# Kernel tuning notes

Hardware: AMD Instinct MI355X
Metric: run time of the kernel (lower is better)

## Reference

```python
import jax, jax.numpy as jnp
import numpy as np

B, S, D = 4, 2048, 2048
H, Dh, Dl = 16, 128, 128  # head_dim must equal latent_dim for the source matmul to type-check


def setup_inputs() -> dict:
    key = jax.random.key(0)
    ks = jax.random.split(key, 6)
    sc = 0.02
    return {
        "hidden_states": jax.random.normal(ks[0], (B, S, D), dtype=jnp.float32),
        "Wq": jax.random.normal(ks[1], (H * Dh, D), dtype=jnp.float32) * sc,
        "Wk_down": jax.random.normal(ks[2], (H * Dl, D), dtype=jnp.float32) * sc,
        "Wv_down": jax.random.normal(ks[3], (H * Dl, D), dtype=jnp.float32) * sc,
        "Wk_up": jax.random.normal(ks[4], (H * Dh, H * Dl), dtype=jnp.float32) * sc,
        "Wo": jax.random.normal(ks[5], (D, H * Dh), dtype=jnp.float32) * sc,
    }


def reference(hidden_states, Wq, Wk_down, Wv_down, Wk_up, Wo):
    # projections (torch Linear: y = x @ W.T)
    q = (hidden_states @ Wq.T).reshape(B, S, H, Dh).transpose(0, 2, 1, 3)        # [B,H,S,Dh]
    k_lat = (hidden_states @ Wk_down.T).reshape(B, S, H, Dl).transpose(0, 2, 1, 3)  # [B,H,S,Dl]
    v_lat = (hidden_states @ Wv_down.T).reshape(B, S, H, Dl).transpose(0, 2, 1, 3)  # [B,H,S,Dl]

    scores = jnp.einsum("bhsd,bhtd->bhst", q, k_lat) / jnp.sqrt(jnp.float32(Dl))
    attn = jax.nn.softmax(scores, axis=-1)
    out_lat = jnp.einsum("bhst,bhtd->bhsd", attn, v_lat)                          # [B,H,S,Dl]
    out_lat = out_lat.transpose(0, 2, 1, 3).reshape(B, S, H * Dl)

    # source bug (faithful): k_up_proj is applied to the attention output
    up = out_lat @ Wk_up.T                                                         # [B,S,H*Dh]
    return up @ Wo.T                                                               # [B,S,D]
```

## Files before the change

kernel.cpp:

```cpp
#include <hip/hip_runtime.h>
#include <hip/hip_bf16.h>
#include <stdint.h>

typedef unsigned short u16;
typedef __attribute__((ext_vector_type(4))) float f32x4;
typedef __attribute__((ext_vector_type(8))) short s16x8;
typedef __attribute__((ext_vector_type(4))) u16 u16x4;

__device__ __forceinline__ u16 f2bf(float x) {
  union { float f; uint32_t u; } v; v.f = x;
  uint32_t r = v.u + 0x7FFFu + ((v.u >> 16) & 1u);
  return (u16)(r >> 16);
}
__device__ __forceinline__ u16 f2bfh(float x) {
  __hip_bfloat16 h = __float2bfloat16(x);
  u16 r; __builtin_memcpy(&r, &h, 2); return r;
}

__device__ __forceinline__ void gload16(const void* g, const void* l) {
  __builtin_amdgcn_global_load_lds((const __attribute__((address_space(1))) void*)g,
                                   (__attribute__((address_space(3))) void*)l,
                                   16, 0, 0);
}

#define BAR() asm volatile("s_barrier" ::: "memory")
#define VMCNT4() asm volatile("s_waitcnt vmcnt(4)" ::: "memory")
#define VMCNT0() asm volatile("s_waitcnt vmcnt(0)" ::: "memory")

__global__ void fill_k(float* out, int n, float v) {
  for (int i = blockIdx.x * blockDim.x + threadIdx.x; i < n; i += gridDim.x * blockDim.x)
    out[i] = v;
}

__global__ void cvtall_k(const float* __restrict__ hs, const float* __restrict__ Wq,
                         const float* __restrict__ Wkd, const float* __restrict__ Wvd,
                         const float* __restrict__ Wo,
                         u16* __restrict__ hsB, u16* __restrict__ W3, u16* __restrict__ WoB) {
  int i = blockIdx.x * blockDim.x + threadIdx.x;
  const float* src; u16* dst; int off;
  if (i < 4194304)      { src = hs;  dst = hsB;          off = i; }
  else if (i < 5242880) { src = Wq;  dst = W3;           off = i - 4194304; }
  else if (i < 6291456) { src = Wkd; dst = W3 + 4194304; off = i - 5242880; }
  else if (i < 7340032) { src = Wvd; dst = W3 + 8388608; off = i - 6291456; }
  else                  { src = Wo;  dst = WoB;          off = i - 7340032; }
  f32x4 v = ((const f32x4*)src)[off];
  u16x4 o;
  o.x = f2bf(v.x); o.y = f2bf(v.y); o.z = f2bf(v.z); o.w = f2bf(v.w);
  ((u16x4*)dst)[off] = o;
}

__global__ void cvtT_k(const float* __restrict__ in, u16* __restrict__ out) {
  __shared__ float t[32][33];
  int tx = threadIdx.x, ty = threadIdx.y;
  int c = blockIdx.x * 32 + tx;
#pragma unroll
  for (int j = 0; j < 4; ++j) {
    int r = blockIdx.y * 32 + ty + j * 8;
    t[ty + j * 8][tx] = in[(size_t)r * 2048 + c];
  }
  __syncthreads();
  int c2 = blockIdx.y * 32 + tx;
#pragma unroll
  for (int j = 0; j < 4; ++j) {
    int r2 = blockIdx.x * 32 + ty + j * 8;
    out[(size_t)r2 * 2048 + c2] = f2bf(t[tx][ty + j * 8]);
  }
}

template <typename CT, int OUTMODE>
__global__ __launch_bounds__(256) void btgemm_k(const u16* __restrict__ A0,
                                                const u16* __restrict__ B0,
                                                CT* __restrict__ C,
                                                int M, int N, int K) {
  __shared__ u16 As[128 * 64];
  __shared__ u16 Bs[128 * 64];
  int nnt = N >> 7;
  int bid = blockIdx.x;
  int nwg = gridDim.x;
  if ((nwg & 7) == 0) { int q = nwg >> 3; bid = (bid & 7) * q + (bid >> 3); }
  int mt = bid / nnt, nt = bid - mt * nnt;
  int tid = threadIdx.x, wave = tid >> 6, lane = tid & 63;
  int l15 = lane & 15, l4 = lane >> 4;
  int wr = wave >> 1, wc = wave & 1;
  int sr = lane >> 3, sc = lane & 7;
  int gsl = (sc ^ sr) * 8;

  const u16* Ag = A0 + (size_t)(mt * 128 + wave * 32 + sr) * K + gsl;
  const u16* Bg = B0 + (size_t)(nt * 128 + wave * 32 + sr) * K + gsl;
  u16* Asw = As + wave * 32 * 64;
  u16* Bsw = Bs + wave * 32 * 64;

  f32x4 acc[4][4];
#pragma unroll
  for (int i = 0; i < 4; ++i)
#pragma unroll
    for (int j = 0; j < 4; ++j) acc[i][j] = f32x4{0.f, 0.f, 0.f, 0.f};

  for (int kt = 0; kt < K; kt += 64) {
#pragma unroll
    for (int i = 0; i < 4; ++i) {
      gload16(Ag + kt + i * 8 * K, Asw + i * 512);
      gload16(Bg + kt + i * 8 * K, Bsw + i * 512);
    }
    __syncthreads();
#pragma unroll
    for (int kk = 0; kk < 2; ++kk) {
      s16x8 af[4], bfr[4];
#pragma unroll
      for (int mf = 0; mf < 4; ++mf) {
        int row = wr * 64 + mf * 16 + l15;
        int sl = ((kk * 4 + l4) ^ (row & 7)) * 8;
        af[mf] = *(const s16x8*)(As + row * 64 + sl);
      }
#pragma unroll
      for (int nf = 0; nf < 4; ++nf) {
        int row = wc * 64 + nf * 16 + l15;
        int sl = ((kk * 4 + l4) ^ (row & 7)) * 8;
        bfr[nf] = *(const s16x8*)(Bs + row * 64 + sl);
      }
#pragma unroll
      for (int mf = 0; mf < 4; ++mf)
#pragma unroll
        for (int nf = 0; nf < 4; ++nf)
          acc[mf][nf] = __builtin_amdgcn_mfma_f32_16x16x32_bf16(af[mf], bfr[nf], acc[mf][nf], 0, 0, 0);
    }
    __syncthreads();
  }

  int crow = mt * 128 + wr * 64 + l4 * 4;
  int ccol = nt * 128 + wc * 64 + l15;
#pragma unroll
  for (int mf = 0; mf < 4; ++mf)
#pragma unroll
    for (int nf = 0; nf < 4; ++nf)
#pragma unroll
      for (int r = 0; r < 4; ++r) {
        size_t idx = (size_t)(crow + mf * 16 + r) * N + (ccol + nf * 16);
        float v = acc[mf][nf][r];
        if constexpr (OUTMODE == 0) C[idx] = v; else C[idx] = f2bfh(v);
      }
}

template <int NTILES, int OUTM>
__global__ __launch_bounds__(512, 2) void gemm256_k(const u16* __restrict__ A0,
                                                    const u16* __restrict__ B0,
                                                    u16* __restrict__ qk,
                                                    u16* __restrict__ Vt,
                                                    float* __restrict__ C) {
  __shared__ u16 lds4[4][2][8192];

  const int K = 2048;
  int bid = blockIdx.x;
  int bid2 = (bid & 7) * (NTILES * 4) + (bid >> 3);
  int mt = bid2 / NTILES, nt = bid2 - mt * NTILES;
  int tid = threadIdx.x, wave = tid >> 6, lane = tid & 63;
  int l15 = lane & 15, l4 = lane >> 4;
  int wr = wave >> 2, wc = wave & 3;

  int rowin = tid >> 2;
  int gsl = (tid & 3) ^ (rowin & 3) ^ ((rowin >> 2) & 3);
  const u16* Agst = A0 + (size_t)(mt * 256 + rowin) * K + gsl * 8;
  const u16* Bgst = B0 + (size_t)(nt * 256 + rowin) * K + gsl * 8;
  const size_t HSTRIDE = (size_t)128 * K;

  int sl = l4 ^ (l15 & 3) ^ ((l15 >> 2) & 3);
  int aoff = wr * 4096 + l15 * 32 + sl * 8;
  int boff = wc * 2048 + l15 * 32 + sl * 8;

  f32x4 acc[8][4];
#pragma unroll
  for (int i = 0; i < 8; ++i)
#pragma unroll
    for (int j = 0; j < 4; ++j) acc[i][j] = f32x4{0.f, 0.f, 0.f, 0.f};

#pragma unroll
  for (int p = 0; p < 3; ++p) {
    gload16(Agst + p * 32, &lds4[p][0][wave * 512]);
    gload16(Agst + HSTRIDE + p * 32, &lds4[p][0][4096 + wave * 512]);
    gload16(Bgst + p * 32, &lds4[p][1][wave * 512]);
    gload16(Bgst + HSTRIDE + p * 32, &lds4[p][1][4096 + wave * 512]);
  }
  VMCNT4();
  BAR();

  s16x8 afc[4], afn[4], bfr0[4], bfr1[4];
#pragma unroll
  for (int i = 0; i < 4; ++i) {
    afc[i] = *(const s16x8*)(&lds4[0][0][0] + aoff + i * 512);
    bfr0[i] = *(const s16x8*)(&lds4[0][1][0] + boff + i * 512);
  }

#define TILE_STEP(T, BFC, BFN)                                                           \
  {                                                                                      \
    const u16* Ab = lds4[(T) & 3][0];                                                    \
    const u16* Abn = lds4[((T) + 1) & 3][0];                                             \
    const u16* Bbn = lds4[((T) + 1) & 3][1];                                             \
    int tt = ((T) + 3) & 63;                                                             \
    int sb = tt & 3;                                                                     \
    _Pragma("unroll") for (int i = 0; i < 4; ++i)                                        \
      afn[i] = *(const s16x8*)(Ab + aoff + (i + 4) * 512);                               \
    gload16(Agst + tt * 32, &lds4[sb][0][wave * 512]);                                   \
    gload16(Agst + HSTRIDE + tt * 32, &lds4[sb][0][4096 + wave * 512]);                  \
    __builtin_amdgcn_s_setprio(1);                                                       \
    _Pragma("unroll") for (int mf = 0; mf < 4; ++mf)                                     \
      _Pragma("unroll") for (int nf = 0; nf < 4; ++nf)                                   \
        acc[mf][nf] = __builtin_amdgcn_mfma_f32_16x16x32_bf16(afc[mf], BFC[nf],          \
                                                              acc[mf][nf], 0, 0, 0);    \
    __builtin_amdgcn_s_setprio(0);                                                       \
    BAR();                                                                               \
    _Pragma("unroll") for (int i = 0; i < 4; ++i) {                                      \
      afc[i] = *(const s16x8*)(Abn + aoff + i * 512);                                    \
      BFN[i] = *(const s16x8*)(Bbn + boff + i * 512);                                    \
    }                                                                                    \
    gload16(Bgst + tt * 32, &lds4[sb][1][wave * 512]);                                   \
    gload16(Bgst + HSTRIDE + tt * 32, &lds4[sb][1][4096 + wave * 512]);                  \
    __builtin_amdgcn_s_setprio(1);                                                       \
    _Pragma("unroll") for (int mf = 0; mf < 4; ++mf)                                     \
      _Pragma("unroll") for (int nf = 0; nf < 4; ++nf)                                   \
        acc[mf + 4][nf] = __builtin_amdgcn_mfma_f32_16x16x32_bf16(afn[mf], BFC[nf],      \
                                                                  acc[mf + 4][nf], 0, 0, 0); \
    __builtin_amdgcn_s_setprio(0);                                                       \
    VMCNT4();                                                                            \
    BAR();                                                                               \
  }

  for (int t2 = 0; t2 < 32; ++t2) {
    TILE_STEP(2 * t2, bfr0, bfr1)
    TILE_STEP(2 * t2 + 1, bfr1, bfr0)
  }
#undef TILE_STEP
  VMCNT0();

  int crow0 = mt * 256 + wr * 128 + l4 * 4;
  int ccol0 = nt * 256 + wc * 64 + l15;
#pragma unroll
  for (int mf = 0; mf < 8; ++mf)
#pragma unroll
    for (int nf = 0; nf < 4; ++nf) {
      int col = ccol0 + nf * 16;
      int row0 = crow0 + mf * 16;
      if constexpr (OUTM == 1) {
#pragma unroll
        for (int r = 0; r < 4; ++r)
          C[(size_t)(row0 + r) * (NTILES * 256) + col] = acc[mf][nf][r];
      } else {
        if (col >= 4096) {
          int h = (col - 4096) >> 7, dh = (col - 4096) & 127;
          int b = row0 >> 11, s0 = row0 & 2047;
          u16x4 w;
          w.x = f2bfh(acc[mf][nf][0]); w.y = f2bfh(acc[mf][nf][1]);
          w.z = f2bfh(acc[mf][nf][2]); w.w = f2bfh(acc[mf][nf][3]);
          *(u16x4*)(Vt + ((size_t)((b << 4) + h) * 128 + dh) * 2048 + s0) = w;
        } else {
#pragma unroll
          for (int r = 0; r < 4; ++r)
            qk[(size_t)(row0 + r) * 4096 + col] = f2bfh(acc[mf][nf][r]);
        }
      }
    }
}

__global__ __launch_bounds__(512, 4) void attn9_k(const u16* __restrict__ qk,
                                                  const u16* __restrict__ Vt,
                                                  u16* __restrict__ outl) {
  __shared__ u16 Ks[2][64 * 128];
  __shared__ u16 Vs[2][128 * 64];
  __shared__ u16 Ps2[8 * 16 * 64];

  int bid = blockIdx.x;
  int xcd = bid & 7, slot = bid >> 3;
  int bh = xcd * 8 + (slot >> 4), qb = slot & 15;
  int b = bh >> 4, h = bh & 15;
  int tid = threadIdx.x, wave = tid >> 6, lane = tid & 63;
  int l15 = lane & 15, l4 = lane >> 4;
  int q0 = qb * 128 + wave * 16;
  const float ksc = 0.12751743f;

  s16x8 qf[4];
#pragma unroll
  for (int kf = 0; kf < 4; ++kf)
    qf[kf] = *(const s16x8*)(qk + (size_t)(b * 2048 + q0 + l15) * 4096 +
                             h * 128 + kf * 32 + l4 * 8);

  f32x4 po[8];
  float smrun = -1e30f, lrun = 0.f;
#pragma unroll
  for (int n2 = 0; n2 < 8; ++n2) po[n2] = f32x4{0.f, 0.f, 0.f, 0.f};

  char* PsW = (char*)Ps2 + wave * 2048;

  int krow_b = wave * 8;
  int vrow_b = wave * 16;
  int kj = lane & 15;
  int vj = lane & 7;

  s16x8 kr[2], vr[2];
#define GLOAD_TILE(kv0)                                                                  \
  _Pragma("unroll") for (int i = 0; i < 2; ++i) {                                        \
    int row = krow_b + i * 4 + (lane >> 4);                                              \
    kr[i] = *(const s16x8*)(qk + (size_t)(b * 2048 + (kv0) + row) * 4096 + 2048 +        \
                            h * 128 + kj * 8);                                           \
    int row2 = vrow_b + i * 8 + (lane >> 3);                                             \
    vr[i] = *(const s16x8*)(Vt + (size_t)(bh * 128 + row2) * 2048 + (kv0) + vj * 8);     \
  }

  GLOAD_TILE(0)

  for (int t = 0; t < 32; ++t) {
    int cur = t & 1;
    u16* Ksc = Ks[cur];
    u16* Vsc = Vs[cur];
#pragma unroll
    for (int i = 0; i < 2; ++i) {
      int row = krow_b + i * 4 + (lane >> 4);
      *(s16x8*)(Ksc + row * 128 + ((kj ^ (row & 7)) * 8)) = kr[i];
      int row2 = vrow_b + i * 8 + (lane >> 3);
      *(s16x8*)(Vsc + row2 * 64 + ((vj ^ (row2 & 7)) * 8)) = vr[i];
    }
    __syncthreads();
    if (t < 31) GLOAD_TILE((t + 1) * 64)

    f32x4 sa[4];
#pragma unroll
    for (int nf = 0; nf < 4; ++nf) sa[nf] = f32x4{0.f, 0.f, 0.f, 0.f};
    __builtin_amdgcn_s_setprio(1);
#pragma unroll
    for (int kf = 0; kf < 4; ++kf) {
      s16x8 kb[4];
#pragma unroll
      for (int nf = 0; nf < 4; ++nf) {
        int row = nf * 16 + l15;
        int sl = ((kf * 4 + l4) ^ (row & 7)) * 8;
        kb[nf] = *(const s16x8*)(Ksc + row * 128 + sl);
      }
#pragma unroll
      for (int nf = 0; nf < 4; ++nf)
        sa[nf] = __builtin_amdgcn_mfma_f32_16x16x32_bf16(kb[nf], qf[kf], sa[nf], 0, 0, 0);
    }
    __builtin_amdgcn_s_setprio(0);

    {
      float m01 = fmaxf(fmaxf(sa[0][0], sa[0][1]), fmaxf(sa[0][2], sa[0][3]));
      float m23 = fmaxf(fmaxf(sa[1][0], sa[1][1]), fmaxf(sa[1][2], sa[1][3]));
      float m45 = fmaxf(fmaxf(sa[2][0], sa[2][1]), fmaxf(sa[2][2], sa[2][3]));
      float m67 = fmaxf(fmaxf(sa[3][0], sa[3][1]), fmaxf(sa[3][2], sa[3][3]));
      float pmax = fmaxf(fmaxf(m01, m23), fmaxf(m45, m67));
      pmax = fmaxf(pmax, __shfl_xor(pmax, 16, 64));
      pmax = fmaxf(pmax, __shfl_xor(pmax, 32, 64));
      float smax = pmax * ksc;
      if (!__all(smax - smrun <= 8.0f)) {
        float mnew = fmaxf(smrun, smax);
        float fsc = exp2f(smrun - mnew);
        lrun *= fsc;
#pragma unroll
        for (int n2 = 0; n2 < 8; ++n2)
#pragma unroll
          for (int r = 0; r < 4; ++r) po[n2][r] *= fsc;
        smrun = mnew;
      }
      int row = l15;
      int swz = (row & 7) << 4;
      float ssum = 0.f;
#pragma unroll
      for (int nf = 0; nf < 4; ++nf) {
        float p0 = exp2f(fmaf(sa[nf][0], ksc, -smrun));
        float p1 = exp2f(fmaf(sa[nf][1], ksc, -smrun));
        float p2 = exp2f(fmaf(sa[nf][2], ksc, -smrun));
        float p3 = exp2f(fmaf(sa[nf][3], ksc, -smrun));
        ssum += (p0 + p1) + (p2 + p3);
        u16x4 w;
        w.x = f2bfh(p0); w.y = f2bfh(p1); w.z = f2bfh(p2); w.w = f2bfh(p3);
        *(u16x4*)(PsW + row * 128 + (((nf * 4 + l4) * 8) ^ swz)) = w;
      }
      ssum += __shfl_xor(ssum, 16, 64);
      ssum += __shfl_xor(ssum, 32, 64);
      lrun += ssum;
    }

    s16x8 pb[2];
    {
      int row = l15;
      int swz = (row & 7) << 4;
#pragma unroll
      for (int k2 = 0; k2 < 2; ++k2)
        pb[k2] = *(const s16x8*)(PsW + row * 128 + ((k2 * 64 + l4 * 16) ^ swz));
    }

    __builtin_amdgcn_s_setprio(1);
#pragma unroll
    for (int n2 = 0; n2 < 8; ++n2) {
#pragma unroll
      for (int k2 = 0; k2 < 2; ++k2) {
        int row = n2 * 16 + l15;
        int sl = ((k2 * 4 + l4) ^ (row & 7)) * 8;
        s16x8 vb = *(const s16x8*)(Vsc + row * 64 + sl);
        po[n2] = __builtin_amdgcn_mfma_f32_16x16x32_bf16(vb, pb[k2], po[n2], 0, 0, 0);
      }
    }
    __builtin_amdgcn_s_setprio(0);
  }
#undef GLOAD_TILE

  {
    float inv = 1.0f / lrun;
#pragma unroll
    for (int n2 = 0; n2 < 8; ++n2) {
      u16x4 w;
      w.x = f2bfh(po[n2][0] * inv);
      w.y = f2bfh(po[n2][1] * inv);
      w.z = f2bfh(po[n2][2] * inv);
      w.w = f2bfh(po[n2][3] * inv);
      *(u16x4*)(outl + (size_t)(b * 2048 + q0 + l15) * 2048 + h * 128 + n2 * 16 + l4 * 4) = w;
    }
  }
}

extern "C" void kernel_launch(void* const* d_in, const int* in_sizes, int n_in,
                              void* d_out, int out_size, void* d_ws, size_t ws_size,
                              hipStream_t stream) {
  (void)in_sizes; (void)n_in;
  const float* hs  = (const float*)d_in[0];
  const float* Wq  = (const float*)d_in[1];
  const float* Wkd = (const float*)d_in[2];
  const float* Wvd = (const float*)d_in[3];
  const float* Wku = (const float*)d_in[4];
  const float* Wo  = (const float*)d_in[5];
  float* out = (float*)d_out;
  char* ws = (char*)d_ws;

  if (ws_size < 201326592ull) {
    fill_k<<<4096, 256, 0, stream>>>(out, out_size, 1e9f);
    return;
  }

  u16* W3   = (u16*)(ws);
  u16* WcH  = (u16*)(ws + 25165824);
  u16* hsB  = (u16*)(ws + 33554432);
  u16* outl = (u16*)(ws + 33554432);
  u16* qk   = (u16*)(ws + 67108864);
  u16* WoB  = (u16*)(ws + 134217728);
  u16* WkuT = (u16*)(ws + 142606336);
  u16* Vt   = (u16*)(ws + 167772160);

  cvtall_k<<<32768, 256, 0, stream>>>(hs, Wq, Wkd, Wvd, Wo, hsB, W3, WoB);
  cvtT_k<<<dim3(64, 64), dim3(32, 8), 0, stream>>>(Wku, WkuT);

  btgemm_k<u16, 1><<<256, 256, 0, stream>>>(WoB, WkuT, WcH, 2048, 2048, 2048);

  gemm256_k<24, 0><<<768, 512, 0, stream>>>(hsB, W3, qk, Vt, nullptr);

  attn9_k<<<1024, 512, 0, stream>>>(qk, Vt, outl);

  gemm256_k<8, 1><<<256, 512, 0, stream>>>(outl, WcH, nullptr, nullptr, out);
}
```

Baseline: 518.2 us.

## Fold Wo·Wk_up weight-combine GEMM into the QKV projection launch

Removes the separate 128x128-tile btgemm kernel that computed the combined Wo·Wk_up weight. Its 64 tiles of 256x256 now run as extra workgroups appended per XCD to the QKV projection grid (768→832 blocks), using the faster 256-tile pipelined kernel. This drops a launch and fills the tail of the large GEMM, at the cost of a per-block branch and extra kernel arguments. The softmax row-max reduction is also reordered into 3-input max chains.

```diff
diff --git a/kernel.cpp b/kernel.cpp
--- a/kernel.cpp
+++ b/kernel.cpp
@@ -67,92 +67,33 @@
   }
 }
 
-template <typename CT, int OUTMODE>
-__global__ __launch_bounds__(256) void btgemm_k(const u16* __restrict__ A0,
-                                                const u16* __restrict__ B0,
-                                                CT* __restrict__ C,
-                                                int M, int N, int K) {
-  __shared__ u16 As[128 * 64];
-  __shared__ u16 Bs[128 * 64];
-  int nnt = N >> 7;
-  int bid = blockIdx.x;
-  int nwg = gridDim.x;
-  if ((nwg & 7) == 0) { int q = nwg >> 3; bid = (bid & 7) * q + (bid >> 3); }
-  int mt = bid / nnt, nt = bid - mt * nnt;
-  int tid = threadIdx.x, wave = tid >> 6, lane = tid & 63;
-  int l15 = lane & 15, l4 = lane >> 4;
-  int wr = wave >> 1, wc = wave & 1;
-  int sr = lane >> 3, sc = lane & 7;
-  int gsl = (sc ^ sr) * 8;
-
-  const u16* Ag = A0 + (size_t)(mt * 128 + wave * 32 + sr) * K + gsl;
-  const u16* Bg = B0 + (size_t)(nt * 128 + wave * 32 + sr) * K + gsl;
-  u16* Asw = As + wave * 32 * 64;
-  u16* Bsw = Bs + wave * 32 * 64;
-
-  f32x4 acc[4][4];
-#pragma unroll
-  for (int i = 0; i < 4; ++i)
-#pragma unroll
-    for (int j = 0; j < 4; ++j) acc[i][j] = f32x4{0.f, 0.f, 0.f, 0.f};
-
-  for (int kt = 0; kt < K; kt += 64) {
-#pragma unroll
-    for (int i = 0; i < 4; ++i) {
-      gload16(Ag + kt + i * 8 * K, Asw + i * 512);
-      gload16(Bg + kt + i * 8 * K, Bsw + i * 512);
-    }
-    __syncthreads();
-#pragma unroll
-    for (int kk = 0; kk < 2; ++kk) {
-      s16x8 af[4], bfr[4];
-#pragma unroll
-      for (int mf = 0; mf < 4; ++mf) {
-        int row = wr * 64 + mf * 16 + l15;
-        int sl = ((kk * 4 + l4) ^ (row & 7)) * 8;
-        af[mf] = *(const s16x8*)(As + row * 64 + sl);
-      }
-#pragma unroll
-      for (int nf = 0; nf < 4; ++nf) {
-        int row = wc * 64 + nf * 16 + l15;
-        int sl = ((kk * 4 + l4) ^ (row & 7)) * 8;
-        bfr[nf] = *(const s16x8*)(Bs + row * 64 + sl);
-      }
-#pragma unroll
-      for (int mf = 0; mf < 4; ++mf)
-#pragma unroll
-        for (int nf = 0; nf < 4; ++nf)
-          acc[mf][nf] = __builtin_amdgcn_mfma_f32_16x16x32_bf16(af[mf], bfr[nf], acc[mf][nf], 0, 0, 0);
-    }
-    __syncthreads();
-  }
-
-  int crow = mt * 128 + wr * 64 + l4 * 4;
-  int ccol = nt * 128 + wc * 64 + l15;
-#pragma unroll
-  for (int mf = 0; mf < 4; ++mf)
-#pragma unroll
-    for (int nf = 0; nf < 4; ++nf)
-#pragma unroll
-      for (int r = 0; r < 4; ++r) {
-        size_t idx = (size_t)(crow + mf * 16 + r) * N + (ccol + nf * 16);
-        float v = acc[mf][nf][r];
-        if constexpr (OUTMODE == 0) C[idx] = v; else C[idx] = f2bfh(v);
-      }
-}
-
-template <int NTILES, int OUTM>
-__global__ __launch_bounds__(512, 2) void gemm256_k(const u16* __restrict__ A0,
-                                                    const u16* __restrict__ B0,
+template <int NTILES, int OUTM, int WCB>
+__global__ __launch_bounds__(512, 2) void gemm256_k(const u16* __restrict__ A0i,
+                                                    const u16* __restrict__ B0i,
                                                     u16* __restrict__ qk,
                                                     u16* __restrict__ Vt,
-                                                    float* __restrict__ C) {
+                                                    float* __restrict__ C,
+                                                    const u16* __restrict__ WoB,
+                                                    const u16* __restrict__ WkuT,
+                                                    u16* __restrict__ WcH) {
   __shared__ u16 lds4[4][2][8192];
 
   const int K = 2048;
   int bid = blockIdx.x;
-  int bid2 = (bid & 7) * (NTILES * 4) + (bid >> 3);
-  int mt = bid2 / NTILES, nt = bid2 - mt * NTILES;
+  int xcd = bid & 7, i = bid >> 3;
+  bool isW = false;
+  int mt, nt;
+  const u16 *A0, *B0;
+  if (WCB > 0 && i >= NTILES * 4) {
+    isW = true;
+    int ix = xcd * (WCB / 8) + (i - NTILES * 4);
+    mt = ix >> 3; nt = ix & 7;
+    A0 = WoB; B0 = WkuT;
+  } else {
+    int idx = xcd * (NTILES * 4) + i;
+    mt = idx / NTILES; nt = idx - mt * NTILES;
+    A0 = A0i; B0 = B0i;
+  }
   int tid = threadIdx.x, wave = tid >> 6, lane = tid & 63;
   int l15 = lane & 15, l4 = lane >> 4;
   int wr = wave >> 2, wc = wave & 3;
@@ -169,9 +110,9 @@
 
   f32x4 acc[8][4];
 #pragma unroll
-  for (int i = 0; i < 8; ++i)
-#pragma unroll
-    for (int j = 0; j < 4; ++j) acc[i][j] = f32x4{0.f, 0.f, 0.f, 0.f};
+  for (int i2 = 0; i2 < 8; ++i2)
+#pragma unroll
+    for (int j = 0; j < 4; ++j) acc[i2][j] = f32x4{0.f, 0.f, 0.f, 0.f};
 
 #pragma unroll
   for (int p = 0; p < 3; ++p) {
@@ -185,9 +126,9 @@
 
   s16x8 afc[4], afn[4], bfr0[4], bfr1[4];
 #pragma unroll
-  for (int i = 0; i < 4; ++i) {
-    afc[i] = *(const s16x8*)(&lds4[0][0][0] + aoff + i * 512);
-    bfr0[i] = *(const s16x8*)(&lds4[0][1][0] + boff + i * 512);
+  for (int i2 = 0; i2 < 4; ++i2) {
+    afc[i2] = *(const s16x8*)(&lds4[0][0][0] + aoff + i2 * 512);
+    bfr0[i2] = *(const s16x8*)(&lds4[0][1][0] + boff + i2 * 512);
   }
 
 #define TILE_STEP(T, BFC, BFN)                                                           \
@@ -197,8 +138,8 @@
     const u16* Bbn = lds4[((T) + 1) & 3][1];                                             \
     int tt = ((T) + 3) & 63;                                                             \
     int sb = tt & 3;                                                                     \
-    _Pragma("unroll") for (int i = 0; i < 4; ++i)                                        \
-      afn[i] = *(const s16x8*)(Ab + aoff + (i + 4) * 512);                               \
+    _Pragma("unroll") for (int i3 = 0; i3 < 4; ++i3)                                     \
+      afn[i3] = *(const s16x8*)(Ab + aoff + (i3 + 4) * 512);                             \
     gload16(Agst + tt * 32, &lds4[sb][0][wave * 512]);                                   \
     gload16(Agst + HSTRIDE + tt * 32, &lds4[sb][0][4096 + wave * 512]);                  \
     __builtin_amdgcn_s_setprio(1);                                                       \
@@ -208,9 +149,9 @@
                                                               acc[mf][nf], 0, 0, 0);    \
     __builtin_amdgcn_s_setprio(0);                                                       \
     BAR();                                                                               \
-    _Pragma("unroll") for (int i = 0; i < 4; ++i) {                                      \
-      afc[i] = *(const s16x8*)(Abn + aoff + i * 512);                                    \
-      BFN[i] = *(const s16x8*)(Bbn + boff + i * 512);                                    \
+    _Pragma("unroll") for (int i3 = 0; i3 < 4; ++i3) {                                   \
+      afc[i3] = *(const s16x8*)(Abn + aoff + i3 * 512);                                  \
+      BFN[i3] = *(const s16x8*)(Bbn + boff + i3 * 512);                                  \
     }                                                                                    \
     gload16(Bgst + tt * 32, &lds4[sb][1][wave * 512]);                                   \
     gload16(Bgst + HSTRIDE + tt * 32, &lds4[sb][1][4096 + wave * 512]);                  \
@@ -239,7 +180,11 @@
     for (int nf = 0; nf < 4; ++nf) {
       int col = ccol0 + nf * 16;
       int row0 = crow0 + mf * 16;
-      if constexpr (OUTM == 1) {
+      if (WCB > 0 && isW) {
+#pragma unroll
+        for (int r = 0; r < 4; ++r)
+          WcH[(size_t)(row0 + r) * 2048 + col] = f2bfh(acc[mf][nf][r]);
+      } else if constexpr (OUTM == 1) {
 #pragma unroll
         for (int r = 0; r < 4; ++r)
           C[(size_t)(row0 + r) * (NTILES * 256) + col] = acc[mf][nf][r];
@@ -340,11 +285,14 @@
     __builtin_amdgcn_s_setprio(0);
 
     {
-      float m01 = fmaxf(fmaxf(sa[0][0], sa[0][1]), fmaxf(sa[0][2], sa[0][3]));
-      float m23 = fmaxf(fmaxf(sa[1][0], sa[1][1]), fmaxf(sa[1][2], sa[1][3]));
-      float m45 = fmaxf(fmaxf(sa[2][0], sa[2][1]), fmaxf(sa[2][2], sa[2][3]));
-      float m67 = fmaxf(fmaxf(sa[3][0], sa[3][1]), fmaxf(sa[3][2], sa[3][3]));
-      float pmax = fmaxf(fmaxf(m01, m23), fmaxf(m45, m67));
+      float t0 = fmaxf(fmaxf(sa[0][0], sa[0][1]), sa[0][2]);
+      float t1 = fmaxf(fmaxf(sa[0][3], sa[1][0]), sa[1][1]);
+      float t2 = fmaxf(fmaxf(sa[1][2], sa[1][3]), sa[2][0]);
+      float t3 = fmaxf(fmaxf(sa[2][1], sa[2][2]), sa[2][3]);
+      float t4 = fmaxf(fmaxf(sa[3][0], sa[3][1]), sa[3][2]);
+      float pmax = fmaxf(fmaxf(t0, t1), t2);
+      pmax = fmaxf(fmaxf(pmax, t3), t4);
+      pmax = fmaxf(pmax, sa[3][3]);
       pmax = fmaxf(pmax, __shfl_xor(pmax, 16, 64));
       pmax = fmaxf(pmax, __shfl_xor(pmax, 32, 64));
       float smax = pmax * ksc;
@@ -445,11 +393,10 @@
   cvtall_k<<<32768, 256, 0, stream>>>(hs, Wq, Wkd, Wvd, Wo, hsB, W3, WoB);
   cvtT_k<<<dim3(64, 64), dim3(32, 8), 0, stream>>>(Wku, WkuT);
 
-  btgemm_k<u16, 1><<<256, 256, 0, stream>>>(WoB, WkuT, WcH, 2048, 2048, 2048);
-
-  gemm256_k<24, 0><<<768, 512, 0, stream>>>(hsB, W3, qk, Vt, nullptr);
+  gemm256_k<24, 0, 64><<<832, 512, 0, stream>>>(hsB, W3, qk, Vt, nullptr, WoB, WkuT, WcH);
 
   attn9_k<<<1024, 512, 0, stream>>>(qk, Vt, outl);
 
-  gemm256_k<8, 1><<<256, 512, 0, stream>>>(outl, WcH, nullptr, nullptr, out);
-}
+  gemm256_k<8, 1, 0><<<256, 512, 0, stream>>>(outl, WcH, nullptr, nullptr, out,
+                                              nullptr, nullptr, nullptr);
+}
```

Result: no change. 518.3 us (+0.0%).
